# Kernel tuning notes

Measured on AMD Instinct MI355X. Metric: run time of the kernel, lower is better.

## Reference

```python
import jax, jax.numpy as jnp
import numpy as np

PAD_BIG = 1e20  # matches F.pad(value=1e20) on y2


def setup_inputs() -> dict:
    key = jax.random.key(0)
    k1, k2, k3 = jax.random.split(key, 3)
    N, C, H, W = 2, 256, 96, 96
    x = jax.random.normal(k1, (N, C, H, W), dtype=jnp.float32)
    y = jax.random.normal(k2, (N, C, H, W), dtype=jnp.float32)
    labels = jax.random.randint(k3, (N, 1, H, W), 0, 124, dtype=jnp.int32)
    return {"x": x, "y": y, "labels": labels, "max_distance": 4, "num_class": 124}


def _window_stack(p, md, h, w):
    # p: padded [n, c, h+2*md, w+2*md] -> [n, c, h, w, k*k]; offset order
    # (di-major, dj-minor) matches F.unfold column ordering.
    k = 2 * md + 1
    return jnp.stack(
        [p[:, :, di:di + h, dj:dj + w] for di in range(k) for dj in range(k)],
        axis=-1,
    )


def reference(x, y, labels, max_distance, num_class):
    # x: query embedding [N,C,H,W]; y: prev-frame embedding [N,C,H,W]
    # labels: prev-frame labels [N,1,H,W] int
    n, c, h, w = x.shape
    md = max_distance
    k = 2 * md + 1
    kk = k * k

    x2 = jnp.sum(x * x, axis=1)  # [n,h,w]
    y2 = jnp.sum(y * y, axis=1, keepdims=True)  # [n,1,h,w]

    pad_sp = [(0, 0), (0, 0), (md, md), (md, md)]
    py = jnp.pad(y, pad_sp)                                   # zeros
    py2 = jnp.pad(y2, pad_sp, constant_values=PAD_BIG)
    plab = jnp.pad(labels.astype(jnp.float32), pad_sp, constant_values=-1.0)

    y_off = _window_stack(py, md, h, w)          # [n,c,h,w,kk]
    y2_off = _window_stack(py2, md, h, w)[:, 0]  # [n,h,w,kk]
    lab_off = _window_stack(plab, md, h, w)[:, 0]  # [n,h,w,kk]

    corr = jnp.einsum('nchw,nchwp->nhwp', x, y_off)  # [n,h,w,kk]
    d = x2[..., None] + y2_off - 2.0 * corr
    d = (jax.nn.sigmoid(d) - 0.5) * 2.0              # in (-1, 1)

    gt_ids = jnp.arange(num_class, dtype=jnp.float32)
    # mask: [n,h,w,kk,num_class]; padded label -1 never matches -> fill 1.0
    mask = lab_off[..., None] == gt_ids
    dists = jnp.min(jnp.where(mask, d[..., None], 1.0), axis=3)  # [n,h,w,nc]
    return jnp.transpose(dists, (0, 3, 1, 2))  # [n,num_class,h,w]
```

## Files before the change

kernel.cpp:

```cpp
#include <hip/hip_runtime.h>
#include <stdint.h>

#define Nn 2
#define Cc 256
#define Hh 96
#define Ww 96
#define HW (Hh * Ww)
#define MD 4
#define NC 124
#define TH 4
#define TWD 8
#define NQ (TH * TWD)
#define SH (TH + 2 * MD)
#define SWD (TWD + 2 * MD)
#define NS (SH * SWD)
#define BLK 256
#define NBW (Ww / TWD)
#define NBH (Hh / TH)
#define NBLK (Nn * NBH * NBW)
#define YROW 64
#define XOFF (NS * YROW)
#define BUFSZ (XOFF + NQ * YROW)
#define TBL (NQ * NC)
#define CQ 32

#define PPB 32
#define PBLK (Nn * HW / PPB)

#define TEN_BYTES ((size_t)Nn * CQ * HW * 16)
#define XT_OFF  TEN_BYTES
#define Y2_OFF  (TEN_BYTES * 2)
#define X2_OFF  (Y2_OFF + (size_t)Nn * HW * 4)

typedef short short8 __attribute__((ext_vector_type(8)));
typedef float f32x4 __attribute__((ext_vector_type(4)));

__device__ __forceinline__ unsigned fmap(float f) {
    unsigned b = __float_as_uint(f);
    return (b & 0x80000000u) ? ~b : (b | 0x80000000u);
}
__device__ __forceinline__ float funmap(unsigned u) {
    unsigned b = (u & 0x80000000u) ? (u & 0x7fffffffu) : ~u;
    return __uint_as_float(b);
}
__device__ __forceinline__ int swz(int row, int slot) {
    return row * YROW + ((slot ^ ((row >> 1) & 3)) << 4);
}

__global__ __launch_bounds__(256) void prep_xy(
    const float* __restrict__ x, const float* __restrict__ y,
    uint4* __restrict__ yT, uint4* __restrict__ xT,
    float* __restrict__ y2g, float* __restrict__ x2g)
{
    __shared__ float red[2][8][PPB];
    const int t = threadIdx.x;
    const int bid = blockIdx.x;
    const int n = bid / (HW / PPB);
    const int pix0 = (bid - n * (HW / PPB)) * PPB;
    const int pl  = t & 31;
    const int grp = t >> 5;
    const size_t pbase = (size_t)n * Cc * HW + pix0 + pl;

    float sq[2] = {0.f, 0.f};
#pragma unroll
    for (int i = 0; i < 8; ++i) {
        const int ts = i >> 2;
        const int cq = grp * 4 + (i & 3);
        const float* src = (ts ? x : y) + pbase + (size_t)(cq * 8) * HW;
        float v[8];
#pragma unroll
        for (int j = 0; j < 8; ++j) v[j] = src[(size_t)j * HW];
        float s = 0.f;
        unsigned pk[4];
#pragma unroll
        for (int j = 0; j < 4; ++j) {
            s = fmaf(v[2*j],   v[2*j],   s);
            s = fmaf(v[2*j+1], v[2*j+1], s);
            pk[j] = (__float_as_uint(v[2*j]) >> 16) |
                    (__float_as_uint(v[2*j+1]) & 0xffff0000u);
        }
        sq[ts] += s;
        uint4* dst = (ts ? xT : yT) + ((size_t)n * CQ + cq) * HW + pix0 + pl;
        *dst = make_uint4(pk[0], pk[1], pk[2], pk[3]);
    }
    red[0][grp][pl] = sq[0];
    red[1][grp][pl] = sq[1];
    __syncthreads();
    if (t < 64) {
        const int ts = t >> 5, p = t & 31;
        float s = 0.f;
#pragma unroll
        for (int g = 0; g < 8; ++g) s += red[ts][g][p];
        (ts ? x2g : y2g)[(size_t)n * HW + pix0 + p] = s;
    }
}

__global__ __launch_bounds__(BLK) void propnet_mfma(
    const uint4* __restrict__ yT, const uint4* __restrict__ xT,
    const float* __restrict__ y2g, const float* __restrict__ x2g,
    const int* __restrict__ labels, float* __restrict__ out)
{
    __shared__ __align__(16) unsigned char sbuf[2][BUFSZ];
    __shared__ float y2s[NS];
    __shared__ float x2s[NQ];
    __shared__ int   labs[NS];
    unsigned* table = (unsigned*)&sbuf[0][0];

    const int t = threadIdx.x;

    const int orig = blockIdx.x;
    const int lin  = (orig & 7) * (NBLK / 8) + (orig >> 3);
    const int n    = lin / (NBH * NBW);
    const int rem  = lin - n * (NBH * NBW);
    const int h0   = (rem / NBW) * TH;
    const int w0   = (rem % NBW) * TWD;

    if (t < NS) {
        const int sr = t >> 4, sc = t & 15;
        const int gh = h0 - MD + sr, gw = w0 - MD + sc;
        const bool ok = (gh >= 0) && (gh < Hh) && (gw >= 0) && (gw < Ww);
        labs[t] = ok ? labels[(size_t)n * HW + gh * Ww + gw] : -1;
        y2s[t]  = ok ? y2g[(size_t)n * HW + gh * Ww + gw] : 0.f;
    }
    if (t < NQ) {
        const int qr = t >> 3, qc = t & 7;
        x2s[t] = x2g[(size_t)n * HW + (size_t)(h0 + qr) * Ww + (w0 + qc)];
    }

    const int lane = t & 63;
    const int wid  = t >> 6;

    size_t ysrc[3]; int yl[3];
    {
        const int sc4 = lane >> 2;
        const int pos = lane & 3;
        const int cqw = pos ^ ((sc4 >> 1) & 3);
#pragma unroll
        for (int i = 0; i < 3; ++i) {
            const int g  = wid * 3 + i;
            const int gh = min(max(h0 - MD + g, 0), Hh - 1);
            const int gw = min(max(w0 - MD + sc4, 0), Ww - 1);
            ysrc[i] = (size_t)cqw * HW + (size_t)gh * Ww + gw;
            yl[i]   = g * 1024;
        }
    }
    const bool hasx = (wid < 2);
    size_t xsrc = 0; int xl = 0;
    if (hasx) {
        const int q   = wid * 16 + (lane >> 2);
        const int pos = lane & 3;
        const int s   = pos ^ ((q >> 1) & 3);
        xsrc = (size_t)s * HW + (size_t)(h0 + (q >> 3)) * Ww + (w0 + (q & 7));
        xl   = XOFF + wid * 1024;
    }
    const uint4* yTn = yT + (size_t)n * CQ * HW;
    const uint4* xTn = xT + (size_t)n * CQ * HW;
    auto stage = [&](int b, int c) {
        const uint4* yb = yTn + (size_t)(c * 4) * HW;
#pragma unroll
        for (int i = 0; i < 3; ++i)
            __builtin_amdgcn_global_load_lds(
                (const __attribute__((address_space(1))) unsigned int*)(yb + ysrc[i]),
                (__attribute__((address_space(3))) unsigned int*)(sbuf[b] + yl[i]),
                16, 0, 0);
        if (hasx)
            __builtin_amdgcn_global_load_lds(
                (const __attribute__((address_space(1))) unsigned int*)
                    (xTn + (size_t)(c * 4) * HW + xsrc),
                (__attribute__((address_space(3))) unsigned int*)(sbuf[b] + xl),
                16, 0, 0);
    };

    const int l15 = lane & 15;
    const int lg  = lane >> 4;
    int aoff[2], boff[3];
#pragma unroll
    for (int mf = 0; mf < 2; ++mf) aoff[mf] = XOFF + swz(mf * 16 + l15, lg);
#pragma unroll
    for (int nf = 0; nf < 3; ++nf) boff[nf] = swz(wid * 48 + nf * 16 + l15, lg);

    f32x4 acc[2][3];
#pragma unroll
    for (int mf = 0; mf < 2; ++mf)
#pragma unroll
        for (int nf = 0; nf < 3; ++nf)
            acc[mf][nf] = (f32x4){0.f, 0.f, 0.f, 0.f};

    auto compute = [&](const unsigned char* bb) {
        short8 a[2], b[3];
#pragma unroll
        for (int mf = 0; mf < 2; ++mf) a[mf] = *(const short8*)(bb + aoff[mf]);
#pragma unroll
        for (int nf = 0; nf < 3; ++nf) b[nf] = *(const short8*)(bb + boff[nf]);
#pragma unroll
        for (int mf = 0; mf < 2; ++mf)
#pragma unroll
            for (int nf = 0; nf < 3; ++nf)
                acc[mf][nf] = __builtin_amdgcn_mfma_f32_16x16x32_bf16(
                    a[mf], b[nf], acc[mf][nf], 0, 0, 0);
    };

    stage(0, 0);
    __syncthreads();
    for (int c = 0; c < 8; ++c) {
        const int b = c & 1;
        if (c < 7) stage(b ^ 1, c + 1);
        compute(sbuf[b]);
        __syncthreads();
    }

    for (int i = t; i < TBL; i += BLK) table[i] = 0xBF800000u;
    __syncthreads();

#pragma unroll
    for (int mf = 0; mf < 2; ++mf) {
#pragma unroll
        for (int nf = 0; nf < 3; ++nf) {
#pragma unroll
            for (int r = 0; r < 4; ++r) {
                const int q = mf * 16 + lg * 4 + r;
                const int s = wid * 48 + nf * 16 + l15;
                const int qr = q >> 3, qc = q & 7;
                const int sr = s >> 4, sc = s & 15;
                const int di = sr - qr, dj = sc - qc;
                const int lab = labs[s];
                if (di >= 0 && di <= 2 * MD && dj >= 0 && dj <= 2 * MD &&
                    lab >= 0 && lab < NC) {
                    const float d  = x2s[q] + y2s[s] - 2.0f * acc[mf][nf][r];
                    const float sg = 1.0f / (1.0f + __expf(-d));
                    atomicMin(&table[q * NC + lab], fmap(fmaf(2.0f, sg, -1.0f)));
                }
            }
        }
    }
    __syncthreads();

    const size_t ob = (size_t)n * NC * HW;
    for (int i = t; i < TBL; i += BLK) {
        const int g = i >> 5;
        const int q = i & 31;
        const int qr = q >> 3, qc = q & 7;
        out[ob + (size_t)g * HW + (size_t)(h0 + qr) * Ww + (w0 + qc)] =
            funmap(table[q * NC + g]);
    }
}

extern "C" void kernel_launch(void* const* d_in, const int* in_sizes, int n_in,
                              void* d_out, int out_size, void* d_ws, size_t ws_size,
                              hipStream_t stream) {
    const float* x      = (const float*)d_in[0];
    const float* y      = (const float*)d_in[1];
    const int*   labels = (const int*)d_in[2];
    float*       out    = (float*)d_out;
    uint4* yT  = (uint4*)d_ws;
    uint4* xT  = (uint4*)((char*)d_ws + XT_OFF);
    float* y2g = (float*)((char*)d_ws + Y2_OFF);
    float* x2g = (float*)((char*)d_ws + X2_OFF);
    (void)in_sizes; (void)n_in; (void)out_size; (void)ws_size;

    prep_xy<<<dim3(PBLK), dim3(256), 0, stream>>>(x, y, yT, xT, y2g, x2g);
    propnet_mfma<<<dim3(NBLK), dim3(BLK), 0, stream>>>(yT, xT, y2g, x2g, labels, out);
}
```

Measured before the change: 31.76 us.

## Stage prep transpose through LDS with float4 loads and split norm partials

The prep kernel now loads a 64-channel by 256-pixel tile with coalesced float4 reads into shared memory, then packs bf16 channel octets from LDS. Each block handles one tensor, batch and 64-channel group, writing partial squared norms that the main kernel sums over four groups. The aim is wider, better-coalesced global reads and more parallel blocks in the prep pass. The cost is a 64KB LDS tile per block, which limits occupancy, plus extra partial-norm traffic and adds in the main kernel.

```diff
diff --git a/kernel.cpp b/kernel.cpp
--- a/kernel.cpp
+++ b/kernel.cpp
@@ -24,13 +24,13 @@
 #define TBL (NQ * NC)
 #define CQ 32
 
-#define PPB 32
-#define PBLK (Nn * HW / PPB)
+#define PPX 256
+#define NSTR (HW / PPX)
+#define PBLK (2 * Nn * 4 * NSTR)
 
 #define TEN_BYTES ((size_t)Nn * CQ * HW * 16)
-#define XT_OFF  TEN_BYTES
-#define Y2_OFF  (TEN_BYTES * 2)
-#define X2_OFF  (Y2_OFF + (size_t)Nn * HW * 4)
+#define XT_OFF    TEN_BYTES
+#define PART_OFF  (TEN_BYTES * 2)
 
 typedef short short8 __attribute__((ext_vector_type(8)));
 typedef float f32x4 __attribute__((ext_vector_type(4)));
@@ -47,58 +47,55 @@
     return row * YROW + ((slot ^ ((row >> 1) & 3)) << 4);
 }
 
-__global__ __launch_bounds__(256) void prep_xy(
+__global__ __launch_bounds__(256) void prep_t(
     const float* __restrict__ x, const float* __restrict__ y,
-    uint4* __restrict__ yT, uint4* __restrict__ xT,
-    float* __restrict__ y2g, float* __restrict__ x2g)
+    uint4* __restrict__ yT, uint4* __restrict__ xT, float* __restrict__ parts)
 {
-    __shared__ float red[2][8][PPB];
+    __shared__ float tile[64 * PPX];
     const int t = threadIdx.x;
     const int bid = blockIdx.x;
-    const int n = bid / (HW / PPB);
-    const int pix0 = (bid - n * (HW / PPB)) * PPB;
-    const int pl  = t & 31;
-    const int grp = t >> 5;
-    const size_t pbase = (size_t)n * Cc * HW + pix0 + pl;
-
-    float sq[2] = {0.f, 0.f};
-#pragma unroll
-    for (int i = 0; i < 8; ++i) {
-        const int ts = i >> 2;
-        const int cq = grp * 4 + (i & 3);
-        const float* src = (ts ? x : y) + pbase + (size_t)(cq * 8) * HW;
+    const int strip = bid % NSTR;
+    const int rest  = bid / NSTR;
+    const int g4  = rest & 3;
+    const int n   = (rest >> 2) & 1;
+    const int ten = rest >> 3;
+    const int pix0 = strip * PPX;
+    const float* src = (ten ? x : y) + ((size_t)n * Cc + g4 * 64) * HW + pix0;
+    uint4* dstT = (ten ? xT : yT) + (size_t)n * CQ * HW;
+
+    const int wid = t >> 6, lane = t & 63;
+#pragma unroll
+    for (int k = 0; k < 16; ++k) {
+        const int m = wid * 16 + k;
+        const float4 v = *(const float4*)(src + (size_t)m * HW + lane * 4);
+        *(float4*)&tile[m * PPX + lane * 4] = v;
+    }
+    __syncthreads();
+
+    float sq = 0.f;
+#pragma unroll
+    for (int k = 0; k < 8; ++k) {
         float v[8];
 #pragma unroll
-        for (int j = 0; j < 8; ++j) v[j] = src[(size_t)j * HW];
-        float s = 0.f;
+        for (int j = 0; j < 8; ++j) v[j] = tile[(k * 8 + j) * PPX + t];
         unsigned pk[4];
 #pragma unroll
         for (int j = 0; j < 4; ++j) {
-            s = fmaf(v[2*j],   v[2*j],   s);
-            s = fmaf(v[2*j+1], v[2*j+1], s);
+            sq = fmaf(v[2*j],   v[2*j],   sq);
+            sq = fmaf(v[2*j+1], v[2*j+1], sq);
             pk[j] = (__float_as_uint(v[2*j]) >> 16) |
                     (__float_as_uint(v[2*j+1]) & 0xffff0000u);
         }
-        sq[ts] += s;
-        uint4* dst = (ts ? xT : yT) + ((size_t)n * CQ + cq) * HW + pix0 + pl;
-        *dst = make_uint4(pk[0], pk[1], pk[2], pk[3]);
-    }
-    red[0][grp][pl] = sq[0];
-    red[1][grp][pl] = sq[1];
-    __syncthreads();
-    if (t < 64) {
-        const int ts = t >> 5, p = t & 31;
-        float s = 0.f;
-#pragma unroll
-        for (int g = 0; g < 8; ++g) s += red[ts][g][p];
-        (ts ? x2g : y2g)[(size_t)n * HW + pix0 + p] = s;
-    }
+        dstT[(size_t)(g4 * 8 + k) * HW + pix0 + t] =
+            make_uint4(pk[0], pk[1], pk[2], pk[3]);
+    }
+    parts[((size_t)(ten * 4 + g4) * Nn + n) * HW + pix0 + t] = sq;
 }
 
 __global__ __launch_bounds__(BLK) void propnet_mfma(
     const uint4* __restrict__ yT, const uint4* __restrict__ xT,
-    const float* __restrict__ y2g, const float* __restrict__ x2g,
-    const int* __restrict__ labels, float* __restrict__ out)
+    const float* __restrict__ parts, const int* __restrict__ labels,
+    float* __restrict__ out)
 {
     __shared__ __align__(16) unsigned char sbuf[2][BUFSZ];
     __shared__ float y2s[NS];
@@ -115,16 +112,28 @@
     const int h0   = (rem / NBW) * TH;
     const int w0   = (rem % NBW) * TWD;
 
+    const float* ypart = parts;
+    const float* xpart = parts + (size_t)4 * Nn * HW;
+
     if (t < NS) {
         const int sr = t >> 4, sc = t & 15;
         const int gh = h0 - MD + sr, gw = w0 - MD + sc;
         const bool ok = (gh >= 0) && (gh < Hh) && (gw >= 0) && (gw < Ww);
         labs[t] = ok ? labels[(size_t)n * HW + gh * Ww + gw] : -1;
-        y2s[t]  = ok ? y2g[(size_t)n * HW + gh * Ww + gw] : 0.f;
+        float s = 0.f;
+        if (ok) {
+            const size_t idx = (size_t)n * HW + gh * Ww + gw;
+#pragma unroll
+            for (int g = 0; g < 4; ++g) s += ypart[(size_t)g * Nn * HW + idx];
+        }
+        y2s[t] = s;
     }
     if (t < NQ) {
-        const int qr = t >> 3, qc = t & 7;
-        x2s[t] = x2g[(size_t)n * HW + (size_t)(h0 + qr) * Ww + (w0 + qc)];
+        const size_t idx = (size_t)n * HW + (size_t)(h0 + (t >> 3)) * Ww + (w0 + (t & 7));
+        float s = 0.f;
+#pragma unroll
+        for (int g = 0; g < 4; ++g) s += xpart[(size_t)g * Nn * HW + idx];
+        x2s[t] = s;
     }
 
     const int lane = t & 63;
@@ -252,12 +261,11 @@
     const float* y      = (const float*)d_in[1];
     const int*   labels = (const int*)d_in[2];
     float*       out    = (float*)d_out;
-    uint4* yT  = (uint4*)d_ws;
-    uint4* xT  = (uint4*)((char*)d_ws + XT_OFF);
-    float* y2g = (float*)((char*)d_ws + Y2_OFF);
-    float* x2g = (float*)((char*)d_ws + X2_OFF);
+    uint4* yT    = (uint4*)d_ws;
+    uint4* xT    = (uint4*)((char*)d_ws + XT_OFF);
+    float* parts = (float*)((char*)d_ws + PART_OFF);
     (void)in_sizes; (void)n_in; (void)out_size; (void)ws_size;
 
-    prep_xy<<<dim3(PBLK), dim3(256), 0, stream>>>(x, y, yT, xT, y2g, x2g);
-    propnet_mfma<<<dim3(NBLK), dim3(BLK), 0, stream>>>(yT, xT, y2g, x2g, labels, out);
-}
+    prep_t<<<dim3(PBLK), dim3(256), 0, stream>>>(x, y, yT, xT, parts);
+    propnet_mfma<<<dim3(NBLK), dim3(BLK), 0, stream>>>(yT, xT, parts, labels, out);
+}
```

After: 32.16 us. No clear change (+1.3%).
